# Kernel tuning notes

Hardware: AMD Instinct MI355X
Metric: run time of the kernel (lower is better)

The kernel has to match this reference:

```python
import jax, jax.numpy as jnp
import numpy as np

N = 100000   # num nodes
E = 1200000  # num edges (avg degree ~12)
D = 64       # emb_dim


def setup_inputs() -> dict:
    key = jax.random.key(0)
    k1, k2, k3, k4, k5, k6 = jax.random.split(key, 6)
    x = jax.random.normal(k1, (N, D), dtype=jnp.float32)
    edge_index = jax.random.randint(k2, (2, E), 0, N, dtype=jnp.int64)
    edge_attr = jax.random.normal(k3, (E, D), dtype=jnp.float32)
    W = jax.random.normal(k4, (D, D), dtype=jnp.float32) * 0.05  # Linear weight
    b = jax.random.normal(k5, (D,), dtype=jnp.float32) * 0.05    # Linear bias
    root_emb = jax.random.normal(k6, (D,), dtype=jnp.float32)
    return {"x": x, "edge_index": edge_index, "edge_attr": edge_attr,
            "W": W, "b": b, "root_emb": root_emb}


def reference(x, edge_index, edge_attr, W, b, root_emb):
    n = x.shape[0]
    x = x @ W.T + b  # Linear(emb_dim, emb_dim)
    row, col = edge_index[0], edge_index[1]
    ones_e = jnp.ones(row.shape[0], dtype=x.dtype)
    # degrees initialized to ones then index_add of ones per edge endpoint
    deg_i = 1.0 + jax.ops.segment_sum(ones_e, row, num_segments=n)
    deg_j = 1.0 + jax.ops.segment_sum(ones_e, col, num_segments=n)
    dinv_i = deg_i ** -0.5
    dinv_j = deg_j ** -0.5
    val = dinv_i[row] * dinv_j[col]  # [E] normalized edge weights
    # spmm(adj_t, x) + message_edge both scatter val-weighted terms to `row`;
    # fuse into a single gather->scale->segment_sum pass (identical math).
    agg = jax.ops.segment_sum(val[:, None] * (x[col] + edge_attr), row,
                              num_segments=n)  # [N, D]
    node_feat = jax.nn.relu(agg) + jax.nn.relu(x + root_emb) * (dinv_i * dinv_j)[:, None]
    return node_feat
```

## Files before the change

kernel.cpp:

```cpp
#include <hip/hip_runtime.h>

#define N_NODES 100000
#define N_EDGES 1200000
#define DIM     64
#define SCAN_B  256
#define NB      ((N_NODES + SCAN_B - 1) / SCAN_B)

typedef unsigned short ushort_t;

__device__ inline float bf2f(ushort_t u) {
    return __uint_as_float(((unsigned int)u) << 16);
}
__device__ inline ushort_t f2bf(float f) {
    unsigned int x = __float_as_uint(f);
    unsigned int r = x + 0x7fff + ((x >> 16) & 1);
    return (ushort_t)(r >> 16);
}

__global__ __launch_bounds__(256) void linear_kernel(
        const float* __restrict__ x, const float* __restrict__ W,
        const float* __restrict__ b, ushort_t* __restrict__ xwb) {
    __shared__ float sWt[DIM * (DIM + 1)];
    __shared__ float sx[16][DIM];

    int t = threadIdx.x;
    int row0 = blockIdx.x * 16;

    for (int i = t; i < DIM * DIM; i += 256) {
        int d = i >> 6, k = i & 63;
        sWt[k * (DIM + 1) + d] = W[i];
    }
    {
        int lr = t >> 4, off = (t & 15) << 2;
        const float4 v = *(const float4*)(x + (size_t)(row0 + lr) * DIM + off);
        sx[lr][off + 0] = v.x; sx[lr][off + 1] = v.y;
        sx[lr][off + 2] = v.z; sx[lr][off + 3] = v.w;
    }
    __syncthreads();

    int d      = t & 63;
    int waveId = t >> 6;
    int r0     = waveId * 4;

    float bd = b[d];
    float a0 = bd, a1 = bd, a2 = bd, a3 = bd;
    const float2* x0 = (const float2*)sx[r0 + 0];
    const float2* x1 = (const float2*)sx[r0 + 1];
    const float2* x2 = (const float2*)sx[r0 + 2];
    const float2* x3 = (const float2*)sx[r0 + 3];
    #pragma unroll
    for (int k2 = 0; k2 < DIM / 2; k2++) {
        float w0 = sWt[(2 * k2 + 0) * (DIM + 1) + d];
        float w1 = sWt[(2 * k2 + 1) * (DIM + 1) + d];
        float2 v0 = x0[k2], v1 = x1[k2], v2 = x2[k2], v3 = x3[k2];
        a0 = fmaf(v0.x, w0, a0); a0 = fmaf(v0.y, w1, a0);
        a1 = fmaf(v1.x, w0, a1); a1 = fmaf(v1.y, w1, a1);
        a2 = fmaf(v2.x, w0, a2); a2 = fmaf(v2.y, w1, a2);
        a3 = fmaf(v3.x, w0, a3); a3 = fmaf(v3.y, w1, a3);
    }
    size_t base = (size_t)(row0 + r0) * DIM + d;
    xwb[base + 0 * DIM] = f2bf(a0);
    xwb[base + 1 * DIM] = f2bf(a1);
    xwb[base + 2 * DIM] = f2bf(a2);
    xwb[base + 3 * DIM] = f2bf(a3);
}

__global__ void count_kernel(const int* __restrict__ row, const int* __restrict__ col,
                             int* __restrict__ cnt_r, int* __restrict__ cnt_c) {
    int i = blockIdx.x * blockDim.x + threadIdx.x;
    if (i * 4 >= N_EDGES) return;
    int4 r4 = ((const int4*)row)[i];
    int4 c4 = ((const int4*)col)[i];
    atomicAdd(&cnt_r[r4.x], 1); atomicAdd(&cnt_r[r4.y], 1);
    atomicAdd(&cnt_r[r4.z], 1); atomicAdd(&cnt_r[r4.w], 1);
    atomicAdd(&cnt_c[c4.x], 1); atomicAdd(&cnt_c[c4.y], 1);
    atomicAdd(&cnt_c[c4.z], 1); atomicAdd(&cnt_c[c4.w], 1);
}

__global__ void scan_a(const int* __restrict__ cnt_r, const int* __restrict__ cnt_c,
                       int* __restrict__ offsets, int* __restrict__ partials,
                       float* __restrict__ dinv_i, float* __restrict__ dinv_j) {
    __shared__ int s[SCAN_B];
    int t = threadIdx.x;
    int i = blockIdx.x * SCAN_B + t;
    int v = (i < N_NODES) ? cnt_r[i] : 0;
    if (i < N_NODES) {
        dinv_i[i] = rsqrtf(1.0f + (float)v);
        dinv_j[i] = rsqrtf(1.0f + (float)cnt_c[i]);
    }
    s[t] = v;
    __syncthreads();
    for (int off = 1; off < SCAN_B; off <<= 1) {
        int add = (t >= off) ? s[t - off] : 0;
        __syncthreads();
        s[t] += add;
        __syncthreads();
    }
    if (i < N_NODES) offsets[i] = s[t] - v;
    if (t == SCAN_B - 1) partials[blockIdx.x] = s[t];
}

__global__ void scan_b(int* __restrict__ partials) {
    __shared__ int s[512];
    int t = threadIdx.x;
    int v = (t < NB) ? partials[t] : 0;
    s[t] = v;
    __syncthreads();
    for (int off = 1; off < 512; off <<= 1) {
        int add = (t >= off) ? s[t - off] : 0;
        __syncthreads();
        s[t] += add;
        __syncthreads();
    }
    if (t < NB) partials[t] = s[t] - v;
}

__global__ void scan_c(int* __restrict__ offsets, const int* __restrict__ partials,
                       int* __restrict__ cursor) {
    int i = blockIdx.x * SCAN_B + threadIdx.x;
    if (i < N_NODES) {
        int o = offsets[i] + partials[blockIdx.x];
        offsets[i] = o;
        cursor[i]  = o;
    }
}

__global__ void bin_kernel(const int* __restrict__ row, const int* __restrict__ col,
                           const float* __restrict__ dinv_i,
                           const float* __restrict__ dinv_j,
                           int* __restrict__ cursor,
                           int2* __restrict__ rec, float* __restrict__ valr) {
    int e = blockIdx.x * blockDim.x + threadIdx.x;
    if (e >= N_EDGES) return;
    int r = row[e], c = col[e];
    int pos = atomicAdd(&cursor[r], 1);
    rec[pos]  = make_int2(e, c);
    valr[pos] = dinv_i[r] * dinv_j[c];
}

__global__ __launch_bounds__(256) void gather_kernel(
        const int* __restrict__ offsets, const int* __restrict__ cnt_r,
        const int2* __restrict__ rec, const float* __restrict__ valr,
        const float* __restrict__ edge_attr, const ushort_t* __restrict__ xwb,
        const float* __restrict__ dinv_i, const float* __restrict__ dinv_j,
        const float* __restrict__ root, float* __restrict__ out) {
    int lane = threadIdx.x & 63;
    int g    = lane >> 4;
    int q    = (lane & 15) << 2;
    int n    = blockIdx.x * 4 + (threadIdx.x >> 6);

    int start = offsets[n];
    int cnt   = cnt_r[n];

    float4 acc = make_float4(0.f, 0.f, 0.f, 0.f);
    int k = g;
    if (k < cnt) {
        int2  rc = rec[start + k];
        float vv = valr[start + k];
        while (true) {
            int  kn   = k + 4;
            bool more = kn < cnt;
            int2 rcn; float vvn;
            if (more) { rcn = rec[start + kn]; vvn = valr[start + kn]; }
            const float4  ea = *(const float4*)(edge_attr + (size_t)rc.x * DIM + q);
            const ushort4 xu = *(const ushort4*)(xwb + (size_t)rc.y * DIM + q);
            acc.x = fmaf(vv, ea.x + bf2f(xu.x), acc.x);
            acc.y = fmaf(vv, ea.y + bf2f(xu.y), acc.y);
            acc.z = fmaf(vv, ea.z + bf2f(xu.z), acc.z);
            acc.w = fmaf(vv, ea.w + bf2f(xu.w), acc.w);
            if (!more) break;
            k = kn; rc = rcn; vv = vvn;
        }
    }

    acc.x += __shfl_xor(acc.x, 16); acc.y += __shfl_xor(acc.y, 16);
    acc.z += __shfl_xor(acc.z, 16); acc.w += __shfl_xor(acc.w, 16);
    acc.x += __shfl_xor(acc.x, 32); acc.y += __shfl_xor(acc.y, 32);
    acc.z += __shfl_xor(acc.z, 32); acc.w += __shfl_xor(acc.w, 32);

    if ((lane >> 4) == 0) {
        float s = dinv_i[n] * dinv_j[n];
        const ushort4 xu = *(const ushort4*)(xwb + (size_t)n * DIM + q);
        const float4  rt = *(const float4*)(root + q);
        float4 o;
        o.x = fmaxf(acc.x, 0.f) + fmaxf(bf2f(xu.x) + rt.x, 0.f) * s;
        o.y = fmaxf(acc.y, 0.f) + fmaxf(bf2f(xu.y) + rt.y, 0.f) * s;
        o.z = fmaxf(acc.z, 0.f) + fmaxf(bf2f(xu.z) + rt.z, 0.f) * s;
        o.w = fmaxf(acc.w, 0.f) + fmaxf(bf2f(xu.w) + rt.w, 0.f) * s;
        *(float4*)(out + (size_t)n * DIM + q) = o;
    }
}

extern "C" void kernel_launch(void* const* d_in, const int* in_sizes, int n_in,
                              void* d_out, int out_size, void* d_ws, size_t ws_size,
                              hipStream_t stream) {
    const float* x         = (const float*)d_in[0];
    const int*   edge_idx  = (const int*)d_in[1];
    const float* edge_attr = (const float*)d_in[2];
    const float* W         = (const float*)d_in[3];
    const float* b         = (const float*)d_in[4];
    const float* root_emb  = (const float*)d_in[5];
    float*       out       = (float*)d_out;

    const int* row = edge_idx;
    const int* col = edge_idx + N_EDGES;

    char* ws = (char*)d_ws;
    ushort_t* xwb      = (ushort_t*)ws;   ws += (size_t)N_NODES * DIM * 2;
    int*      cnt_r    = (int*)ws;        ws += (size_t)N_NODES * 4;
    int*      cnt_c    = (int*)ws;        ws += (size_t)N_NODES * 4;
    float*    dinv_i   = (float*)ws;      ws += (size_t)N_NODES * 4;
    float*    dinv_j   = (float*)ws;      ws += (size_t)N_NODES * 4;
    int*      offsets  = (int*)ws;        ws += (size_t)N_NODES * 4;
    int*      cursor   = (int*)ws;        ws += (size_t)N_NODES * 4;
    int*      partials = (int*)ws;        ws += 1024 * 4;
    int2*     rec      = (int2*)ws;       ws += (size_t)N_EDGES * 8;
    float*    valr     = (float*)ws;      ws += (size_t)N_EDGES * 4;

    hipMemsetAsync(cnt_r, 0, (size_t)N_NODES * 2 * sizeof(int), stream);

    linear_kernel<<<N_NODES / 16, 256, 0, stream>>>(x, W, b, xwb);

    count_kernel<<<(N_EDGES / 4 + 255) / 256, 256, 0, stream>>>(row, col, cnt_r, cnt_c);

    scan_a<<<NB, SCAN_B, 0, stream>>>(cnt_r, cnt_c, offsets, partials, dinv_i, dinv_j);
    scan_b<<<1, 512, 0, stream>>>(partials);
    scan_c<<<NB, SCAN_B, 0, stream>>>(offsets, partials, cursor);

    bin_kernel<<<(N_EDGES + 255) / 256, 256, 0, stream>>>(
        row, col, dinv_i, dinv_j, cursor, rec, valr);

    gather_kernel<<<N_NODES / 4, 256, 0, stream>>>(
        offsets, cnt_r, rec, valr, edge_attr, xwb, dinv_i, dinv_j, root_emb, out);
}
```

Baseline: 666.0 us.

## Drop per-edge weight array, fold scan_b into scan_c, prefetch gather loads

```diff
diff --git a/kernel.cpp b/kernel.cpp
--- a/kernel.cpp
+++ b/kernel.cpp
@@ -38,9 +38,8 @@
     }
     __syncthreads();
 
-    int d      = t & 63;
-    int waveId = t >> 6;
-    int r0     = waveId * 4;
+    int d  = t & 63;
+    int r0 = (t >> 6) * 4;
 
     float bd = b[d];
     float a0 = bd, a1 = bd, a2 = bd, a3 = bd;
@@ -100,47 +99,40 @@
     if (t == SCAN_B - 1) partials[blockIdx.x] = s[t];
 }
 
-__global__ void scan_b(int* __restrict__ partials) {
-    __shared__ int s[512];
-    int t = threadIdx.x;
-    int v = (t < NB) ? partials[t] : 0;
-    s[t] = v;
-    __syncthreads();
-    for (int off = 1; off < 512; off <<= 1) {
-        int add = (t >= off) ? s[t - off] : 0;
-        __syncthreads();
-        s[t] += add;
-        __syncthreads();
-    }
-    if (t < NB) partials[t] = s[t] - v;
-}
-
 __global__ void scan_c(int* __restrict__ offsets, const int* __restrict__ partials,
                        int* __restrict__ cursor) {
-    int i = blockIdx.x * SCAN_B + threadIdx.x;
+    __shared__ int sred[SCAN_B];
+    int t = threadIdx.x, bid = blockIdx.x;
+    int v = 0;
+    for (int j = t; j < NB; j += SCAN_B)
+        if (j < bid) v += partials[j];
+    sred[t] = v;
+    __syncthreads();
+    for (int off = SCAN_B / 2; off > 0; off >>= 1) {
+        if (t < off) sred[t] += sred[t + off];
+        __syncthreads();
+    }
+    int base = sred[0];
+    int i = bid * SCAN_B + t;
     if (i < N_NODES) {
-        int o = offsets[i] + partials[blockIdx.x];
+        int o = offsets[i] + base;
         offsets[i] = o;
         cursor[i]  = o;
     }
 }
 
 __global__ void bin_kernel(const int* __restrict__ row, const int* __restrict__ col,
-                           const float* __restrict__ dinv_i,
-                           const float* __restrict__ dinv_j,
-                           int* __restrict__ cursor,
-                           int2* __restrict__ rec, float* __restrict__ valr) {
+                           int* __restrict__ cursor, int2* __restrict__ rec) {
     int e = blockIdx.x * blockDim.x + threadIdx.x;
     if (e >= N_EDGES) return;
     int r = row[e], c = col[e];
     int pos = atomicAdd(&cursor[r], 1);
-    rec[pos]  = make_int2(e, c);
-    valr[pos] = dinv_i[r] * dinv_j[c];
+    rec[pos] = make_int2(e, c);
 }
 
 __global__ __launch_bounds__(256) void gather_kernel(
         const int* __restrict__ offsets, const int* __restrict__ cnt_r,
-        const int2* __restrict__ rec, const float* __restrict__ valr,
+        const int2* __restrict__ rec,
         const float* __restrict__ edge_attr, const ushort_t* __restrict__ xwb,
         const float* __restrict__ dinv_i, const float* __restrict__ dinv_j,
         const float* __restrict__ root, float* __restrict__ out) {
@@ -149,27 +141,34 @@
     int q    = (lane & 15) << 2;
     int n    = blockIdx.x * 4 + (threadIdx.x >> 6);
 
-    int start = offsets[n];
-    int cnt   = cnt_r[n];
+    int   start = offsets[n];
+    int   cnt   = cnt_r[n];
+    float di    = dinv_i[n];
 
     float4 acc = make_float4(0.f, 0.f, 0.f, 0.f);
     int k = g;
     if (k < cnt) {
-        int2  rc = rec[start + k];
-        float vv = valr[start + k];
-        while (true) {
+        int2    rc = rec[start + k];
+        float4  ea = *(const float4*)(edge_attr + (size_t)rc.x * DIM + q);
+        ushort4 xu = *(const ushort4*)(xwb + (size_t)rc.y * DIM + q);
+        float   vj = dinv_j[rc.y];
+        for (;;) {
             int  kn   = k + 4;
             bool more = kn < cnt;
-            int2 rcn; float vvn;
-            if (more) { rcn = rec[start + kn]; vvn = valr[start + kn]; }
-            const float4  ea = *(const float4*)(edge_attr + (size_t)rc.x * DIM + q);
-            const ushort4 xu = *(const ushort4*)(xwb + (size_t)rc.y * DIM + q);
+            int2 rcn; float4 ean; ushort4 xun; float vjn;
+            if (more) {
+                rcn = rec[start + kn];
+                ean = *(const float4*)(edge_attr + (size_t)rcn.x * DIM + q);
+                xun = *(const ushort4*)(xwb + (size_t)rcn.y * DIM + q);
+                vjn = dinv_j[rcn.y];
+            }
+            float vv = di * vj;
             acc.x = fmaf(vv, ea.x + bf2f(xu.x), acc.x);
             acc.y = fmaf(vv, ea.y + bf2f(xu.y), acc.y);
             acc.z = fmaf(vv, ea.z + bf2f(xu.z), acc.z);
             acc.w = fmaf(vv, ea.w + bf2f(xu.w), acc.w);
             if (!more) break;
-            k = kn; rc = rcn; vv = vvn;
+            k = kn; ea = ean; xu = xun; vj = vjn;
         }
     }
 
@@ -178,8 +177,8 @@
     acc.x += __shfl_xor(acc.x, 32); acc.y += __shfl_xor(acc.y, 32);
     acc.z += __shfl_xor(acc.z, 32); acc.w += __shfl_xor(acc.w, 32);
 
-    if ((lane >> 4) == 0) {
-        float s = dinv_i[n] * dinv_j[n];
+    if (g == 0) {
+        float s = di * dinv_j[n];
         const ushort4 xu = *(const ushort4*)(xwb + (size_t)n * DIM + q);
         const float4  rt = *(const float4*)(root + q);
         float4 o;
@@ -215,7 +214,6 @@
     int*      cursor   = (int*)ws;        ws += (size_t)N_NODES * 4;
     int*      partials = (int*)ws;        ws += 1024 * 4;
     int2*     rec      = (int2*)ws;       ws += (size_t)N_EDGES * 8;
-    float*    valr     = (float*)ws;      ws += (size_t)N_EDGES * 4;
 
     hipMemsetAsync(cnt_r, 0, (size_t)N_NODES * 2 * sizeof(int), stream);
 
@@ -224,12 +222,10 @@
     count_kernel<<<(N_EDGES / 4 + 255) / 256, 256, 0, stream>>>(row, col, cnt_r, cnt_c);
 
     scan_a<<<NB, SCAN_B, 0, stream>>>(cnt_r, cnt_c, offsets, partials, dinv_i, dinv_j);
-    scan_b<<<1, 512, 0, stream>>>(partials);
     scan_c<<<NB, SCAN_B, 0, stream>>>(offsets, partials, cursor);
 
-    bin_kernel<<<(N_EDGES + 255) / 256, 256, 0, stream>>>(
-        row, col, dinv_i, dinv_j, cursor, rec, valr);
+    bin_kernel<<<(N_EDGES + 255) / 256, 256, 0, stream>>>(row, col, cursor, rec);
 
     gather_kernel<<<N_NODES / 4, 256, 0, stream>>>(
-        offsets, cnt_r, rec, valr, edge_attr, xwb, dinv_i, dinv_j, root_emb, out);
-}
+        offsets, cnt_r, rec, edge_attr, xwb, dinv_i, dinv_j, root_emb, out);
+}
```

Result: no change. 675.6 us (+1.4%).
